# Kernel optimization log

Hardware: AMD Instinct MI355X
Metric: run time of the kernel (lower is better)

The kernel has to match this reference:

```python
import jax, jax.numpy as jnp
import numpy as np

N = 50000          # nodes
E = 800000         # edges (avg degree 16)
INPUT_DIM = 1024
K = 10             # conv1d kernel
STRIDE = 8
COUT = (INPUT_DIM - K) // STRIDE + 1   # 127, matches floor formula
H = 256            # hidden_dim


def setup_inputs() -> dict:
    key = jax.random.key(0)
    ks = jax.random.split(key, 12)
    sc = lambda k, s: (jax.random.normal(k, s, jnp.float32) * 0.05)
    inp = {}
    inp["h"] = jax.random.normal(ks[0], (N, INPUT_DIM), jnp.float32)
    inp["src"] = jax.random.randint(ks[1], (E,), 0, N, dtype=jnp.int32)
    inp["dst"] = jax.random.randint(ks[2], (E,), 0, N, dtype=jnp.int32)
    # Conv1d(1,1,k=10,stride=8)
    inp["conv1d_w"] = sc(ks[3], (1, 1, K))
    inp["conv1d_b"] = jnp.zeros((1,), jnp.float32)
    # SAGEConv1: 127 -> 256 (mean aggregator: fc_self + fc_neigh)
    inp["w_self1"] = sc(ks[4], (COUT, H))
    inp["w_neigh1"] = sc(ks[5], (COUT, H))
    inp["b1"] = jnp.zeros((H,), jnp.float32)
    # SAGEConv2: 256 -> 128
    inp["w_self2"] = sc(ks[6], (H, H // 2))
    inp["w_neigh2"] = sc(ks[7], (H, H // 2))
    inp["b2"] = jnp.zeros((H // 2,), jnp.float32)
    # MLP head 128 -> 64 -> 32 -> 1
    inp["fc1_w"] = sc(ks[8], (H // 2, H // 4)); inp["fc1_b"] = jnp.zeros((H // 4,), jnp.float32)
    inp["fc2_w"] = sc(ks[9], (H // 4, H // 8)); inp["fc2_b"] = jnp.zeros((H // 8,), jnp.float32)
    inp["fc3_w"] = sc(ks[10], (H // 8, 1));    inp["fc3_b"] = jnp.zeros((1,), jnp.float32)
    return inp


def _sage_mean(x, src, dst, w_self, w_neigh, b):
    # mean over in-neighbors (src -> dst), zero for isolated nodes (DGL semantics)
    ones = jnp.ones((src.shape[0],), x.dtype)
    deg = jax.ops.segment_sum(ones, dst, num_segments=N)          # [N]
    agg = jax.ops.segment_sum(x[src], dst, num_segments=N)        # [N, F]
    agg = agg / jnp.maximum(deg, 1.0)[:, None]
    return x @ w_self + agg @ w_neigh + b


def reference(h, src, dst, conv1d_w, conv1d_b,
              w_self1, w_neigh1, b1, w_self2, w_neigh2, b2,
              fc1_w, fc1_b, fc2_w, fc2_b, fc3_w, fc3_b):
    # per-node 1D conv over feature axis: [N,1,1024] -> [N,1,127]
    x = jax.lax.conv_general_dilated(h[:, None, :], conv1d_w, (STRIDE,), 'VALID',
                                     dimension_numbers=('NCH', 'OIH', 'NCH'))
    x = jax.nn.relu(x[:, 0, :] + conv1d_b)                        # [N, 127]
    x = jax.nn.relu(_sage_mean(x, src, dst, w_self1, w_neigh1, b1))  # [N, 256]
    x = jax.nn.relu(_sage_mean(x, src, dst, w_self2, w_neigh2, b2))  # [N, 128]
    hg = jnp.mean(x, axis=0, keepdims=True)                       # AvgPooling -> [1, 128]
    y = jax.nn.relu(hg @ fc1_w + fc1_b)
    y = jax.nn.relu(y @ fc2_w + fc2_b)
    return y @ fc3_w + fc3_b                                      # [1, 1]
```

## Files before the change

### kernel.cpp

```cpp
#include <hip/hip_runtime.h>

#define N_NODES 50000
#define N_EDGES 800000
#define IN_DIM  1024
#define COUT    127
#define H1      256
#define H2      128
#define LDA     256
#define MBLK    391
#define NPART   4096
#define LDSS    72

typedef __bf16 bf16;
typedef __attribute__((ext_vector_type(8))) __bf16 bf16x8;
typedef __attribute__((ext_vector_type(4))) float floatx4;

__global__ void conv_kernel(const float* __restrict__ h, const float* __restrict__ w,
                            const float* __restrict__ b, bf16* __restrict__ xa) {
    int n = blockIdx.x;
    int t = threadIdx.x;
    const float* hr = h + (size_t)n * IN_DIM;
    float r = 0.f;
    if (t < COUT) {
        const float* p = hr + t * 8;
        float4 a = *(const float4*)p;
        float4 c = *(const float4*)(p + 4);
        float2 d = *(const float2*)(p + 8);
        float s = b[0];
        s += a.x * w[0] + a.y * w[1] + a.z * w[2] + a.w * w[3];
        s += c.x * w[4] + c.y * w[5] + c.z * w[6] + c.w * w[7];
        s += d.x * w[8] + d.y * w[9];
        r = fmaxf(s, 0.f);
    }
    xa[(size_t)n * LDA + t] = (bf16)r;
}

__global__ void deg_kernel(const int* __restrict__ dst, int* __restrict__ deg) {
    int e = blockIdx.x * blockDim.x + threadIdx.x;
    if (e < N_EDGES) atomicAdd(&deg[dst[e]], 1);
}

__global__ __launch_bounds__(1024) void scan_kernel(const int* __restrict__ deg,
                                                    int* __restrict__ rowptr,
                                                    int* __restrict__ cursor) {
    __shared__ int wsum[16];
    __shared__ int carry_s;
    int tid = threadIdx.x;
    int lane = tid & 63, wid = tid >> 6;
    if (tid == 0) carry_s = 0;
    __syncthreads();
    for (int base = 0; base < N_NODES; base += 1024) {
        int i = base + tid;
        int v = (i < N_NODES) ? deg[i] : 0;
        int s = v;
        #pragma unroll
        for (int off = 1; off < 64; off <<= 1) {
            int t = __shfl_up(s, off);
            if (lane >= off) s += t;
        }
        if (lane == 63) wsum[wid] = s;
        __syncthreads();
        if (tid < 16) {
            int ws = wsum[tid];
            #pragma unroll
            for (int off = 1; off < 16; off <<= 1) {
                int t = __shfl_up(ws, off);
                if (tid >= off) ws += t;
            }
            wsum[tid] = ws;
        }
        __syncthreads();
        int wpre = (wid == 0) ? 0 : wsum[wid - 1];
        int excl = carry_s + wpre + (s - v);
        if (i < N_NODES) { rowptr[i] = excl; cursor[i] = excl; }
        int tot = wsum[15];
        __syncthreads();
        if (tid == 0) carry_s += tot;
        __syncthreads();
    }
    if (tid == 0) rowptr[N_NODES] = carry_s;
}

__global__ void fill_kernel(const int* __restrict__ src, const int* __restrict__ dst,
                            int* __restrict__ cursor, int* __restrict__ esrc) {
    int e = blockIdx.x * blockDim.x + threadIdx.x;
    if (e < N_EDGES) {
        int d = dst[e];
        int pos = atomicAdd(&cursor[d], 1);
        esrc[pos] = src[e];
    }
}

__global__ void agg_kernel(bf16* __restrict__ xa, const int* __restrict__ rowptr,
                           const int* __restrict__ esrc) {
    int n = blockIdx.x;
    int f = threadIdx.x;
    int s0 = rowptr[n], s1 = rowptr[n + 1];
    float acc = 0.f;
    int e = s0;
    for (; e + 8 <= s1; e += 8) {
        int i0 = esrc[e],     i1 = esrc[e + 1], i2 = esrc[e + 2], i3 = esrc[e + 3];
        int i4 = esrc[e + 4], i5 = esrc[e + 5], i6 = esrc[e + 6], i7 = esrc[e + 7];
        float v0 = (float)xa[(size_t)i0 * LDA + f];
        float v1 = (float)xa[(size_t)i1 * LDA + f];
        float v2 = (float)xa[(size_t)i2 * LDA + f];
        float v3 = (float)xa[(size_t)i3 * LDA + f];
        float v4 = (float)xa[(size_t)i4 * LDA + f];
        float v5 = (float)xa[(size_t)i5 * LDA + f];
        float v6 = (float)xa[(size_t)i6 * LDA + f];
        float v7 = (float)xa[(size_t)i7 * LDA + f];
        acc += ((v0 + v1) + (v2 + v3)) + ((v4 + v5) + (v6 + v7));
    }
    for (; e < s1; ++e) acc += (float)xa[(size_t)esrc[e] * LDA + f];
    float dnm = (float)max(s1 - s0, 1);
    xa[(size_t)n * LDA + 128 + f] = (bf16)(acc / dnm);
}

__global__ void padw1_kernel(const float* __restrict__ ws, const float* __restrict__ wn,
                             bf16* __restrict__ wt) {
    int i = blockIdx.x * blockDim.x + threadIdx.x;
    int n = i >> 8, k = i & 255;
    float v = 0.f;
    if (k < COUT)                      v = ws[k * H1 + n];
    else if (k >= 128 && k < 128 + COUT) v = wn[(k - 128) * H1 + n];
    wt[i] = (bf16)v;
}

__global__ void padw2_kernel(const float* __restrict__ ws, const float* __restrict__ wn,
                             bf16* __restrict__ wt) {
    int i = blockIdx.x * blockDim.x + threadIdx.x;
    int n = i >> 8, k = i & 255;
    float v = (n < H2) ? ws[k * H2 + n] : wn[k * H2 + (n - H2)];
    wt[i] = (bf16)v;
}

template <bool RELU>
__global__ __launch_bounds__(256) void gemm_mfma(
        const bf16* __restrict__ X, const bf16* __restrict__ WT,
        const float* __restrict__ bias, bf16* __restrict__ out) {
    __shared__ bf16 As[128 * LDSS];
    __shared__ bf16 Bs[64 * LDSS];
    int tid  = threadIdx.x;
    int lane = tid & 63, w = tid >> 6;
    int quad = lane >> 4, l16 = lane & 15;
    int m0 = blockIdx.x * 128;
    int n0 = blockIdx.y * 64;
    floatx4 acc[2][4] = {};

    for (int k0 = 0; k0 < 256; k0 += 64) {
        uint4 av[4], bv[2];
        #pragma unroll
        for (int i = 0; i < 4; ++i) {
            int c = tid + 256 * i;
            int row = c >> 3, col = (c & 7) * 8;
            int gr = m0 + row;
            av[i] = (gr < N_NODES) ? *(const uint4*)(X + (size_t)gr * LDA + k0 + col)
                                   : make_uint4(0u, 0u, 0u, 0u);
        }
        #pragma unroll
        for (int i = 0; i < 2; ++i) {
            int c = tid + 256 * i;
            int row = c >> 3, col = (c & 7) * 8;
            bv[i] = *(const uint4*)(WT + (size_t)(n0 + row) * 256 + k0 + col);
        }
        __syncthreads();
        #pragma unroll
        for (int i = 0; i < 4; ++i) {
            int c = tid + 256 * i;
            int row = c >> 3, col = (c & 7) * 8;
            *(uint4*)&As[row * LDSS + col] = av[i];
        }
        #pragma unroll
        for (int i = 0; i < 2; ++i) {
            int c = tid + 256 * i;
            int row = c >> 3, col = (c & 7) * 8;
            *(uint4*)&Bs[row * LDSS + col] = bv[i];
        }
        __syncthreads();

        #pragma unroll
        for (int ks = 0; ks < 2; ++ks) {
            int kin = ks * 32 + quad * 8;
            bf16x8 a0 = *(const bf16x8*)&As[(w * 32 + l16) * LDSS + kin];
            bf16x8 a1 = *(const bf16x8*)&As[(w * 32 + 16 + l16) * LDSS + kin];
            bf16x8 b0 = *(const bf16x8*)&Bs[(l16) * LDSS + kin];
            bf16x8 b1 = *(const bf16x8*)&Bs[(16 + l16) * LDSS + kin];
            bf16x8 b2 = *(const bf16x8*)&Bs[(32 + l16) * LDSS + kin];
            bf16x8 b3 = *(const bf16x8*)&Bs[(48 + l16) * LDSS + kin];
            acc[0][0] = __builtin_amdgcn_mfma_f32_16x16x32_bf16(a0, b0, acc[0][0], 0, 0, 0);
            acc[0][1] = __builtin_amdgcn_mfma_f32_16x16x32_bf16(a0, b1, acc[0][1], 0, 0, 0);
            acc[0][2] = __builtin_amdgcn_mfma_f32_16x16x32_bf16(a0, b2, acc[0][2], 0, 0, 0);
            acc[0][3] = __builtin_amdgcn_mfma_f32_16x16x32_bf16(a0, b3, acc[0][3], 0, 0, 0);
            acc[1][0] = __builtin_amdgcn_mfma_f32_16x16x32_bf16(a1, b0, acc[1][0], 0, 0, 0);
            acc[1][1] = __builtin_amdgcn_mfma_f32_16x16x32_bf16(a1, b1, acc[1][1], 0, 0, 0);
            acc[1][2] = __builtin_amdgcn_mfma_f32_16x16x32_bf16(a1, b2, acc[1][2], 0, 0, 0);
            acc[1][3] = __builtin_amdgcn_mfma_f32_16x16x32_bf16(a1, b3, acc[1][3], 0, 0, 0);
        }
    }

    float bvv[4] = {};
    if constexpr (RELU) {
        #pragma unroll
        for (int nt = 0; nt < 4; ++nt) bvv[nt] = bias[n0 + nt * 16 + l16];
    }
    #pragma unroll
    for (int mt = 0; mt < 2; ++mt) {
        #pragma unroll
        for (int r = 0; r < 4; ++r) {
            int m = m0 + w * 32 + mt * 16 + quad * 4 + r;
            if (m < N_NODES) {
                #pragma unroll
                for (int nt = 0; nt < 4; ++nt) {
                    float v = acc[mt][nt][r];
                    if constexpr (RELU) v = fmaxf(v + bvv[nt], 0.f);
                    out[(size_t)m * LDA + n0 + nt * 16 + l16] = (bf16)v;
                }
            }
        }
    }
}

__global__ __launch_bounds__(128) void agg_epi_kernel(
        const bf16* __restrict__ P, const int* __restrict__ rowptr,
        const int* __restrict__ esrc, const float* __restrict__ b2,
        float* __restrict__ partial) {
    int f = threadIdx.x;
    float bf = b2[f];
    float csum = 0.f;
    for (int n = blockIdx.x; n < N_NODES; n += gridDim.x) {
        int s0 = rowptr[n], s1 = rowptr[n + 1];
        float acc = 0.f;
        int e = s0;
        for (; e + 8 <= s1; e += 8) {
            int i0 = esrc[e],     i1 = esrc[e + 1], i2 = esrc[e + 2], i3 = esrc[e + 3];
            int i4 = esrc[e + 4], i5 = esrc[e + 5], i6 = esrc[e + 6], i7 = esrc[e + 7];
            float v0 = (float)P[(size_t)i0 * LDA + H2 + f];
            float v1 = (float)P[(size_t)i1 * LDA + H2 + f];
            float v2 = (float)P[(size_t)i2 * LDA + H2 + f];
            float v3 = (float)P[(size_t)i3 * LDA + H2 + f];
            float v4 = (float)P[(size_t)i4 * LDA + H2 + f];
            float v5 = (float)P[(size_t)i5 * LDA + H2 + f];
            float v6 = (float)P[(size_t)i6 * LDA + H2 + f];
            float v7 = (float)P[(size_t)i7 * LDA + H2 + f];
            acc += ((v0 + v1) + (v2 + v3)) + ((v4 + v5) + (v6 + v7));
        }
        for (; e < s1; ++e) acc += (float)P[(size_t)esrc[e] * LDA + H2 + f];
        float dnm = (float)max(s1 - s0, 1);
        float y = (float)P[(size_t)n * LDA + f] + acc / dnm + bf;
        csum += fmaxf(y, 0.f);
    }
    partial[(size_t)blockIdx.x * 128 + f] = csum;
}

__global__ __launch_bounds__(256) void reduce_kernel(const float* __restrict__ partial,
                                                     float* __restrict__ hg) {
    int f = blockIdx.x, t = threadIdx.x;
    float s = 0.f;
    for (int i = t; i < NPART; i += 256) s += partial[(size_t)i * 128 + f];
    __shared__ float ls[4];
    #pragma unroll
    for (int off = 32; off >= 1; off >>= 1) s += __shfl_down(s, off);
    if ((t & 63) == 0) ls[t >> 6] = s;
    __syncthreads();
    if (t == 0) hg[f] = (ls[0] + ls[1]) + (ls[2] + ls[3]);
}

__global__ void mlp_kernel(const float* __restrict__ hg,
                           const float* __restrict__ f1w, const float* __restrict__ f1b,
                           const float* __restrict__ f2w, const float* __restrict__ f2b,
                           const float* __restrict__ f3w, const float* __restrict__ f3b,
                           float* __restrict__ out) {
    __shared__ float h0[128], y1[64], y2[32];
    int t = threadIdx.x;
    if (t < 128) h0[t] = hg[t] * (1.0f / N_NODES);
    __syncthreads();
    if (t < 64) {
        float s = f1b[t];
        for (int k = 0; k < 128; ++k) s += h0[k] * f1w[k * 64 + t];
        y1[t] = fmaxf(s, 0.f);
    }
    __syncthreads();
    if (t < 32) {
        float s = f2b[t];
        for (int k = 0; k < 64; ++k) s += y1[k] * f2w[k * 32 + t];
        y2[t] = fmaxf(s, 0.f);
    }
    __syncthreads();
    if (t == 0) {
        float s = f3b[0];
        for (int k = 0; k < 32; ++k) s += y2[k] * f3w[k];
        out[0] = s;
    }
}

extern "C" void kernel_launch(void* const* d_in, const int* in_sizes, int n_in,
                              void* d_out, int out_size, void* d_ws, size_t ws_size,
                              hipStream_t stream) {
    (void)in_sizes; (void)n_in; (void)out_size; (void)ws_size;
    const float* h        = (const float*)d_in[0];
    const int*   src      = (const int*)d_in[1];
    const int*   dst      = (const int*)d_in[2];
    const float* cw       = (const float*)d_in[3];
    const float* cb       = (const float*)d_in[4];
    const float* w_self1  = (const float*)d_in[5];
    const float* w_neigh1 = (const float*)d_in[6];
    const float* b1       = (const float*)d_in[7];
    const float* w_self2  = (const float*)d_in[8];
    const float* w_neigh2 = (const float*)d_in[9];
    const float* b2       = (const float*)d_in[10];
    const float* f1w      = (const float*)d_in[11];
    const float* f1b      = (const float*)d_in[12];
    const float* f2w      = (const float*)d_in[13];
    const float* f2b      = (const float*)d_in[14];
    const float* f3w      = (const float*)d_in[15];
    const float* f3b      = (const float*)d_in[16];
    float* out = (float*)d_out;

    char* ws = (char*)d_ws;
    bf16*  xa    = (bf16*) (ws + 0);
    bf16*  P     = (bf16*) (ws + 0);
    bf16*  x2    = (bf16*) (ws + 25624576);
    bf16*  wt1   = (bf16*) (ws + 51249152);
    bf16*  wt2   = (bf16*) (ws + 51380224);
    int*   deg   = (int*)  (ws + 51511296);
    int*   rowp  = (int*)  (ws + 51711488);
    int*   esrc  = (int*)  (ws + 51911936);
    float* part  = (float*)(ws + 55111936);
    float* hg    = (float*)(ws + 57209088);
    int*   cur   = deg;

    hipMemsetAsync(deg, 0, N_NODES * sizeof(int), stream);

    padw1_kernel<<<256, 256, 0, stream>>>(w_self1, w_neigh1, wt1);
    padw2_kernel<<<256, 256, 0, stream>>>(w_self2, w_neigh2, wt2);
    deg_kernel<<<(N_EDGES + 255) / 256, 256, 0, stream>>>(dst, deg);
    scan_kernel<<<1, 1024, 0, stream>>>(deg, rowp, cur);
    fill_kernel<<<(N_EDGES + 255) / 256, 256, 0, stream>>>(src, dst, cur, esrc);
    conv_kernel<<<N_NODES, 128, 0, stream>>>(h, cw, cb, xa);
    agg_kernel<<<N_NODES, 128, 0, stream>>>(xa, rowp, esrc);
    dim3 g(MBLK, 4);
    gemm_mfma<true><<<g, 256, 0, stream>>>(xa, wt1, b1, x2);
    gemm_mfma<false><<<g, 256, 0, stream>>>(x2, wt2, nullptr, P);
    agg_epi_kernel<<<NPART, 128, 0, stream>>>(P, rowp, esrc, b2, part);
    reduce_kernel<<<128, 256, 0, stream>>>(part, hg);
    mlp_kernel<<<1, 128, 0, stream>>>(hg, f1w, f1b, f2w, f2b, f3w, f3b, out);
}
```

Baseline: 597.9 us.

## Gather neighbor features as packed bf16 pairs per wavefront and parallelize scan

The two neighbor-aggregation kernels now give each node one 64-lane wavefront, and each lane loads a 32-bit word holding two bf16 features, unpacked with bit shifts. Previously a 128-thread block did one bf16 per thread. Four nodes share a 256-thread block, and the epilogue uses 8192 streams with float2 partial writes, so the reduce reads twice as many partials. The single-block scan now has each thread sum a 49-element chunk in registers instead of looping over 1024-wide tiles with repeated barriers. The two weight-padding kernels are merged into one launch. Together these aim to halve gather instruction count, drop scan synchronization and cut launch overhead, at the cost of more register use and a larger partial buffer.

```diff
diff --git a/kernel.cpp b/kernel.cpp
--- a/kernel.cpp
+++ b/kernel.cpp
@@ -8,12 +8,16 @@
 #define H2      128
 #define LDA     256
 #define MBLK    391
-#define NPART   4096
+#define NSTREAM 8192
 #define LDSS    72
+#define SCHUNK  49
 
 typedef __bf16 bf16;
 typedef __attribute__((ext_vector_type(8))) __bf16 bf16x8;
 typedef __attribute__((ext_vector_type(4))) float floatx4;
+
+__device__ __forceinline__ float bfu_lo(unsigned u) { return __uint_as_float(u << 16); }
+__device__ __forceinline__ float bfu_hi(unsigned u) { return __uint_as_float(u & 0xffff0000u); }
 
 __global__ void conv_kernel(const float* __restrict__ h, const float* __restrict__ w,
                             const float* __restrict__ b, bf16* __restrict__ xa) {
@@ -43,42 +47,45 @@
 __global__ __launch_bounds__(1024) void scan_kernel(const int* __restrict__ deg,
                                                     int* __restrict__ rowptr,
                                                     int* __restrict__ cursor) {
+    int t = threadIdx.x;
+    int base = t * SCHUNK;
+    int v[SCHUNK];
+    int sum = 0;
+    #pragma unroll
+    for (int i = 0; i < SCHUNK; ++i) {
+        int idx = base + i;
+        v[i] = (idx < N_NODES) ? deg[idx] : 0;
+        sum += v[i];
+    }
     __shared__ int wsum[16];
-    __shared__ int carry_s;
-    int tid = threadIdx.x;
-    int lane = tid & 63, wid = tid >> 6;
-    if (tid == 0) carry_s = 0;
-    __syncthreads();
-    for (int base = 0; base < N_NODES; base += 1024) {
-        int i = base + tid;
-        int v = (i < N_NODES) ? deg[i] : 0;
-        int s = v;
-        #pragma unroll
-        for (int off = 1; off < 64; off <<= 1) {
-            int t = __shfl_up(s, off);
-            if (lane >= off) s += t;
-        }
-        if (lane == 63) wsum[wid] = s;
-        __syncthreads();
-        if (tid < 16) {
-            int ws = wsum[tid];
-            #pragma unroll
-            for (int off = 1; off < 16; off <<= 1) {
-                int t = __shfl_up(ws, off);
-                if (tid >= off) ws += t;
-            }
-            wsum[tid] = ws;
-        }
-        __syncthreads();
-        int wpre = (wid == 0) ? 0 : wsum[wid - 1];
-        int excl = carry_s + wpre + (s - v);
-        if (i < N_NODES) { rowptr[i] = excl; cursor[i] = excl; }
-        int tot = wsum[15];
-        __syncthreads();
-        if (tid == 0) carry_s += tot;
-        __syncthreads();
-    }
-    if (tid == 0) rowptr[N_NODES] = carry_s;
+    int lane = t & 63, wid = t >> 6;
+    int s = sum;
+    #pragma unroll
+    for (int off = 1; off < 64; off <<= 1) {
+        int q = __shfl_up(s, off);
+        if (lane >= off) s += q;
+    }
+    if (lane == 63) wsum[wid] = s;
+    __syncthreads();
+    if (t < 16) {
+        int ws = wsum[t];
+        #pragma unroll
+        for (int off = 1; off < 16; off <<= 1) {
+            int q = __shfl_up(ws, off);
+            if (t >= off) ws += q;
+        }
+        wsum[t] = ws;
+    }
+    __syncthreads();
+    int excl = ((wid == 0) ? 0 : wsum[wid - 1]) + (s - sum);
+    int run = excl;
+    #pragma unroll
+    for (int i = 0; i < SCHUNK; ++i) {
+        int idx = base + i;
+        if (idx < N_NODES) { rowptr[idx] = run; cursor[idx] = run; }
+        run += v[i];
+    }
+    if (t == 1023) rowptr[N_NODES] = run;
 }
 
 __global__ void fill_kernel(const int* __restrict__ src, const int* __restrict__ dst,
@@ -91,47 +98,56 @@
     }
 }
 
-__global__ void agg_kernel(bf16* __restrict__ xa, const int* __restrict__ rowptr,
-                           const int* __restrict__ esrc) {
-    int n = blockIdx.x;
-    int f = threadIdx.x;
+__global__ __launch_bounds__(256) void agg_kernel(bf16* __restrict__ xa,
+                                                  const int* __restrict__ rowptr,
+                                                  const int* __restrict__ esrc) {
+    int w = threadIdx.x >> 6, lane = threadIdx.x & 63;
+    int n = blockIdx.x * 4 + w;
+    const unsigned* base = (const unsigned*)xa;
     int s0 = rowptr[n], s1 = rowptr[n + 1];
-    float acc = 0.f;
+    float a0 = 0.f, a1 = 0.f;
     int e = s0;
     for (; e + 8 <= s1; e += 8) {
-        int i0 = esrc[e],     i1 = esrc[e + 1], i2 = esrc[e + 2], i3 = esrc[e + 3];
-        int i4 = esrc[e + 4], i5 = esrc[e + 5], i6 = esrc[e + 6], i7 = esrc[e + 7];
-        float v0 = (float)xa[(size_t)i0 * LDA + f];
-        float v1 = (float)xa[(size_t)i1 * LDA + f];
-        float v2 = (float)xa[(size_t)i2 * LDA + f];
-        float v3 = (float)xa[(size_t)i3 * LDA + f];
-        float v4 = (float)xa[(size_t)i4 * LDA + f];
-        float v5 = (float)xa[(size_t)i5 * LDA + f];
-        float v6 = (float)xa[(size_t)i6 * LDA + f];
-        float v7 = (float)xa[(size_t)i7 * LDA + f];
-        acc += ((v0 + v1) + (v2 + v3)) + ((v4 + v5) + (v6 + v7));
-    }
-    for (; e < s1; ++e) acc += (float)xa[(size_t)esrc[e] * LDA + f];
+        unsigned u0 = base[(size_t)esrc[e]     * 128 + lane];
+        unsigned u1 = base[(size_t)esrc[e + 1] * 128 + lane];
+        unsigned u2 = base[(size_t)esrc[e + 2] * 128 + lane];
+        unsigned u3 = base[(size_t)esrc[e + 3] * 128 + lane];
+        unsigned u4 = base[(size_t)esrc[e + 4] * 128 + lane];
+        unsigned u5 = base[(size_t)esrc[e + 5] * 128 + lane];
+        unsigned u6 = base[(size_t)esrc[e + 6] * 128 + lane];
+        unsigned u7 = base[(size_t)esrc[e + 7] * 128 + lane];
+        a0 += ((bfu_lo(u0) + bfu_lo(u1)) + (bfu_lo(u2) + bfu_lo(u3)))
+            + ((bfu_lo(u4) + bfu_lo(u5)) + (bfu_lo(u6) + bfu_lo(u7)));
+        a1 += ((bfu_hi(u0) + bfu_hi(u1)) + (bfu_hi(u2) + bfu_hi(u3)))
+            + ((bfu_hi(u4) + bfu_hi(u5)) + (bfu_hi(u6) + bfu_hi(u7)));
+    }
+    for (; e < s1; ++e) {
+        unsigned u = base[(size_t)esrc[e] * 128 + lane];
+        a0 += bfu_lo(u);  a1 += bfu_hi(u);
+    }
     float dnm = (float)max(s1 - s0, 1);
-    xa[(size_t)n * LDA + 128 + f] = (bf16)(acc / dnm);
-}
-
-__global__ void padw1_kernel(const float* __restrict__ ws, const float* __restrict__ wn,
-                             bf16* __restrict__ wt) {
+    bf16 b0 = (bf16)(a0 / dnm), b1 = (bf16)(a1 / dnm);
+    ushort2 pk;
+    pk.x = *(unsigned short*)&b0;  pk.y = *(unsigned short*)&b1;
+    *(ushort2*)&xa[(size_t)n * LDA + 128 + lane * 2] = pk;
+}
+
+__global__ void padw_kernel(const float* __restrict__ ws1, const float* __restrict__ wn1,
+                            const float* __restrict__ ws2, const float* __restrict__ wn2,
+                            bf16* __restrict__ wt1, bf16* __restrict__ wt2) {
     int i = blockIdx.x * blockDim.x + threadIdx.x;
-    int n = i >> 8, k = i & 255;
-    float v = 0.f;
-    if (k < COUT)                      v = ws[k * H1 + n];
-    else if (k >= 128 && k < 128 + COUT) v = wn[(k - 128) * H1 + n];
-    wt[i] = (bf16)v;
-}
-
-__global__ void padw2_kernel(const float* __restrict__ ws, const float* __restrict__ wn,
-                             bf16* __restrict__ wt) {
-    int i = blockIdx.x * blockDim.x + threadIdx.x;
-    int n = i >> 8, k = i & 255;
-    float v = (n < H2) ? ws[k * H2 + n] : wn[k * H2 + (n - H2)];
-    wt[i] = (bf16)v;
+    if (i < 65536) {
+        int n = i >> 8, k = i & 255;
+        float v = 0.f;
+        if (k < COUT)                        v = ws1[k * H1 + n];
+        else if (k >= 128 && k < 128 + COUT) v = wn1[(k - 128) * H1 + n];
+        wt1[i] = (bf16)v;
+    } else {
+        int j = i - 65536;
+        int n = j >> 8, k = j & 255;
+        float v = (n < H2) ? ws2[k * H2 + n] : wn2[k * H2 + (n - H2)];
+        wt2[j] = (bf16)v;
+    }
 }
 
 template <bool RELU>
@@ -220,43 +236,54 @@
     }
 }
 
-__global__ __launch_bounds__(128) void agg_epi_kernel(
+__global__ __launch_bounds__(256) void agg_epi_kernel(
         const bf16* __restrict__ P, const int* __restrict__ rowptr,
         const int* __restrict__ esrc, const float* __restrict__ b2,
         float* __restrict__ partial) {
-    int f = threadIdx.x;
-    float bf = b2[f];
-    float csum = 0.f;
-    for (int n = blockIdx.x; n < N_NODES; n += gridDim.x) {
+    int w = threadIdx.x >> 6, lane = threadIdx.x & 63;
+    int sid = blockIdx.x * 4 + w;
+    int f0 = lane * 2;
+    float bf0 = b2[f0], bf1 = b2[f0 + 1];
+    const unsigned* base = (const unsigned*)P;
+    float cs0 = 0.f, cs1 = 0.f;
+    for (int n = sid; n < N_NODES; n += NSTREAM) {
         int s0 = rowptr[n], s1 = rowptr[n + 1];
-        float acc = 0.f;
+        float a0 = 0.f, a1 = 0.f;
         int e = s0;
         for (; e + 8 <= s1; e += 8) {
-            int i0 = esrc[e],     i1 = esrc[e + 1], i2 = esrc[e + 2], i3 = esrc[e + 3];
-            int i4 = esrc[e + 4], i5 = esrc[e + 5], i6 = esrc[e + 6], i7 = esrc[e + 7];
-            float v0 = (float)P[(size_t)i0 * LDA + H2 + f];
-            float v1 = (float)P[(size_t)i1 * LDA + H2 + f];
-            float v2 = (float)P[(size_t)i2 * LDA + H2 + f];
-            float v3 = (float)P[(size_t)i3 * LDA + H2 + f];
-            float v4 = (float)P[(size_t)i4 * LDA + H2 + f];
-            float v5 = (float)P[(size_t)i5 * LDA + H2 + f];
-            float v6 = (float)P[(size_t)i6 * LDA + H2 + f];
-            float v7 = (float)P[(size_t)i7 * LDA + H2 + f];
-            acc += ((v0 + v1) + (v2 + v3)) + ((v4 + v5) + (v6 + v7));
-        }
-        for (; e < s1; ++e) acc += (float)P[(size_t)esrc[e] * LDA + H2 + f];
+            unsigned u0 = base[(size_t)esrc[e]     * 128 + 64 + lane];
+            unsigned u1 = base[(size_t)esrc[e + 1] * 128 + 64 + lane];
+            unsigned u2 = base[(size_t)esrc[e + 2] * 128 + 64 + lane];
+            unsigned u3 = base[(size_t)esrc[e + 3] * 128 + 64 + lane];
+            unsigned u4 = base[(size_t)esrc[e + 4] * 128 + 64 + lane];
+            unsigned u5 = base[(size_t)esrc[e + 5] * 128 + 64 + lane];
+            unsigned u6 = base[(size_t)esrc[e + 6] * 128 + 64 + lane];
+            unsigned u7 = base[(size_t)esrc[e + 7] * 128 + 64 + lane];
+            a0 += ((bfu_lo(u0) + bfu_lo(u1)) + (bfu_lo(u2) + bfu_lo(u3)))
+                + ((bfu_lo(u4) + bfu_lo(u5)) + (bfu_lo(u6) + bfu_lo(u7)));
+            a1 += ((bfu_hi(u0) + bfu_hi(u1)) + (bfu_hi(u2) + bfu_hi(u3)))
+                + ((bfu_hi(u4) + bfu_hi(u5)) + (bfu_hi(u6) + bfu_hi(u7)));
+        }
+        for (; e < s1; ++e) {
+            unsigned u = base[(size_t)esrc[e] * 128 + 64 + lane];
+            a0 += bfu_lo(u);  a1 += bfu_hi(u);
+        }
         float dnm = (float)max(s1 - s0, 1);
-        float y = (float)P[(size_t)n * LDA + f] + acc / dnm + bf;
-        csum += fmaxf(y, 0.f);
-    }
-    partial[(size_t)blockIdx.x * 128 + f] = csum;
+        unsigned us = base[(size_t)n * 128 + lane];
+        float y0 = bfu_lo(us) + a0 / dnm + bf0;
+        float y1 = bfu_hi(us) + a1 / dnm + bf1;
+        cs0 += fmaxf(y0, 0.f);
+        cs1 += fmaxf(y1, 0.f);
+    }
+    float2 o;  o.x = cs0;  o.y = cs1;
+    *(float2*)&partial[(size_t)sid * 128 + f0] = o;
 }
 
 __global__ __launch_bounds__(256) void reduce_kernel(const float* __restrict__ partial,
                                                      float* __restrict__ hg) {
     int f = blockIdx.x, t = threadIdx.x;
     float s = 0.f;
-    for (int i = t; i < NPART; i += 256) s += partial[(size_t)i * 128 + f];
+    for (int i = t; i < NSTREAM; i += 256) s += partial[(size_t)i * 128 + f];
     __shared__ float ls[4];
     #pragma unroll
     for (int off = 32; off >= 1; off >>= 1) s += __shfl_down(s, off);
@@ -326,22 +353,21 @@
     int*   rowp  = (int*)  (ws + 51711488);
     int*   esrc  = (int*)  (ws + 51911936);
     float* part  = (float*)(ws + 55111936);
-    float* hg    = (float*)(ws + 57209088);
+    float* hg    = (float*)(ws + 59306240);
     int*   cur   = deg;
 
     hipMemsetAsync(deg, 0, N_NODES * sizeof(int), stream);
 
-    padw1_kernel<<<256, 256, 0, stream>>>(w_self1, w_neigh1, wt1);
-    padw2_kernel<<<256, 256, 0, stream>>>(w_self2, w_neigh2, wt2);
+    padw_kernel<<<512, 256, 0, stream>>>(w_self1, w_neigh1, w_self2, w_neigh2, wt1, wt2);
     deg_kernel<<<(N_EDGES + 255) / 256, 256, 0, stream>>>(dst, deg);
     scan_kernel<<<1, 1024, 0, stream>>>(deg, rowp, cur);
     fill_kernel<<<(N_EDGES + 255) / 256, 256, 0, stream>>>(src, dst, cur, esrc);
     conv_kernel<<<N_NODES, 128, 0, stream>>>(h, cw, cb, xa);
-    agg_kernel<<<N_NODES, 128, 0, stream>>>(xa, rowp, esrc);
+    agg_kernel<<<12500, 256, 0, stream>>>(xa, rowp, esrc);
     dim3 g(MBLK, 4);
     gemm_mfma<true><<<g, 256, 0, stream>>>(xa, wt1, b1, x2);
     gemm_mfma<false><<<g, 256, 0, stream>>>(x2, wt2, nullptr, P);
-    agg_epi_kernel<<<NPART, 128, 0, stream>>>(P, rowp, esrc, b2, part);
+    agg_epi_kernel<<<NSTREAM / 4, 256, 0, stream>>>(P, rowp, esrc, b2, part);
     reduce_kernel<<<128, 256, 0, stream>>>(part, hg);
     mlp_kernel<<<1, 128, 0, stream>>>(hg, f1w, f1b, f2w, f2b, f3w, f3b, out);
 }
```

After: 626.9 us. +4.8%, slower.
